# Performance work log

Hardware: AMD Instinct MI355X
Metric: run time of the kernel (lower is better)

## Reference

```python
import jax, jax.numpy as jnp
from jax import lax
import numpy as np

# Straight-through-estimator sign (standard BNN binarization):
# fwd: sign(x) with sign(0)=+1; bwd: pass gradient where |x|<=1 (hardtanh STE).
@jax.custom_vjp
def sign_ste(x):
    return jnp.where(x >= 0, 1.0, -1.0).astype(x.dtype)

def _sign_fwd(x):
    return sign_ste(x), x

def _sign_bwd(x, g):
    return (g * (jnp.abs(x) <= 1.0).astype(g.dtype),)

sign_ste.defvjp(_sign_fwd, _sign_bwd)

EPS = 1e-5  # BatchNorm eps (torch default)

def bn4(x, g, b):  # BatchNorm2d, training-mode batch stats, x: [N,C,H,W]
    m = x.mean((0, 2, 3), keepdims=True)
    v = x.var((0, 2, 3), keepdims=True)
    return g[None, :, None, None] * (x - m) * lax.rsqrt(v + EPS) + b[None, :, None, None]

def bn1(x, g, b):  # BatchNorm1d, x: [N,C]
    m = x.mean(0, keepdims=True)
    v = x.var(0, keepdims=True)
    return g * (x - m) * lax.rsqrt(v + EPS) + b

def bconv(x, W, b, first):
    # BinarizedConv2d: binarize weights always; binarize input except first layer.
    xb = x if first else sign_ste(x)
    y = lax.conv_general_dilated(xb, sign_ste(W), (1, 1), [(1, 1), (1, 1)],
                                 dimension_numbers=('NCHW', 'OIHW', 'NCHW'))
    return y + b[None, :, None, None]

def maxpool2(x):
    return lax.reduce_window(x, -jnp.inf, lax.max, (1, 1, 2, 2), (1, 1, 2, 2), 'VALID')

def ht(x):  # Hardtanh
    return jnp.clip(x, -1.0, 1.0)

CONV_CH = [(3, 64), (64, 128), (128, 256), (256, 256), (256, 512), (512, 512), (512, 512), (512, 512)]
LIN_CH = [(512, 512), (512, 512), (512, 10)]
POOL_AFTER = (0, 1, 3, 5, 7)  # conv indices followed by MaxPool2d

def setup_inputs():
    key = jax.random.key(0)
    ks = iter(jax.random.split(key, 64))
    d = {"x": jax.random.normal(next(ks), (256, 3, 32, 32), jnp.float32)}
    for i, (ci, co) in enumerate(CONV_CH):
        d[f"cw{i}"] = jax.random.normal(next(ks), (co, ci, 3, 3), jnp.float32) * 0.1
        d[f"cb{i}"] = jnp.zeros((co,), jnp.float32)
        d[f"cg{i}"] = jnp.ones((co,), jnp.float32)
        d[f"ct{i}"] = jnp.zeros((co,), jnp.float32)
    for i, (ci, co) in enumerate(LIN_CH):
        d[f"lw{i}"] = jax.random.normal(next(ks), (co, ci), jnp.float32) * 0.1
        d[f"lb{i}"] = jnp.zeros((co,), jnp.float32)
        d[f"lg{i}"] = jnp.ones((co,), jnp.float32)
        d[f"lt{i}"] = jnp.zeros((co,), jnp.float32)
    return d

def _forward(x, cw, cb, cg, ct, lw, lb, lg, lt):
    h = x
    for i in range(8):
        h = bconv(h, cw[i], cb[i], i == 0)
        if i in POOL_AFTER:
            h = maxpool2(h)
        h = ht(bn4(h, cg[i], ct[i]))
    h = h.reshape(h.shape[0], -1)  # [N, 512] after 5 pools on 32x32
    for i in range(3):
        h = sign_ste(h) @ sign_ste(lw[i]).T + lb[i]  # BinarizedLinear
        h = bn1(h, lg[i], lt[i])
        if i < 2:
            h = ht(h)  # Dropout is identity in eval mode
    return jax.nn.log_softmax(h, axis=-1)

def reference(x,
              cw0, cb0, cg0, ct0, cw1, cb1, cg1, ct1, cw2, cb2, cg2, ct2,
              cw3, cb3, cg3, ct3, cw4, cb4, cg4, ct4, cw5, cb5, cg5, ct5,
              cw6, cb6, cg6, ct6, cw7, cb7, cg7, ct7,
              lw0, lb0, lg0, lt0, lw1, lb1, lg1, lt1, lw2, lb2, lg2, lt2):
    cw = [cw0, cw1, cw2, cw3, cw4, cw5, cw6, cw7]
    cb = [cb0, cb1, cb2, cb3, cb4, cb5, cb6, cb7]
    cg = [cg0, cg1, cg2, cg3, cg4, cg5, cg6, cg7]
    ct = [ct0, ct1, ct2, ct3, ct4, ct5, ct6, ct7]
    lw = [lw0, lw1, lw2]
    lb = [lb0, lb1, lb2]
    lg = [lg0, lg1, lg2]
    lt = [lt0, lt1, lt2]
    return _forward(x, cw, cb, cg, ct, lw, lb, lg, lt)
```

## Files before the change

### kernel.cpp

```cpp
#include <hip/hip_runtime.h>
#include <hip/hip_bf16.h>

typedef unsigned long long u64;

#define EPSV 1e-5

__device__ __forceinline__ int imax(int a, int b) { return a > b ? a : b; }
__device__ __forceinline__ int iclamp(int v, int lo, int hi) { return v < lo ? lo : (v > hi ? hi : v); }

struct PrepArgs {
    const float* src[10];
    u64* dst[10];
    int CW[10];
    int Co[10];
    int taps[10];
    int rowbase[11];
    u64* accs;
    int naccs;
};

__global__ __launch_bounds__(256) void prep_kernel(PrepArgs a) {
    __shared__ float buf[4608];
    const int blk = blockIdx.x;
    int z = blk * 18 + threadIdx.x;
    if (threadIdx.x < 18 && z < a.naccs) a.accs[z] = 0ULL;

    int l = 0;
    while (l < 9 && blk >= a.rowbase[l + 1]) ++l;
    const int row = blk - a.rowbase[l];
    const int CW = a.CW[l];
    const int taps = a.taps[l];
    const int nf = CW * 64 * taps;
    const float* srow = a.src[l] + (size_t)row * nf;
    for (int i = threadIdx.x; i < nf; i += 256) buf[i] = srow[i];
    __syncthreads();
    const int t = threadIdx.x;
    if (t < taps * CW) {
        u64 bits = 0;
        if (taps == 9) {
            int k = t % 9, w = t / 9;
            for (int j = 0; j < 64; ++j) bits |= (u64)(buf[(w * 64 + j) * 9 + k] >= 0.f) << j;
            a.dst[l][(size_t)(k * CW + w) * a.Co[l] + row] = bits;
        } else {
            for (int j = 0; j < 64; ++j) bits |= (u64)(buf[t * 64 + j] >= 0.f) << j;
            a.dst[l][(size_t)row * CW + t] = bits;
        }
    }
}

__global__ __launch_bounds__(256) void conv0_lane(const float* __restrict__ x,
                                                  const float* __restrict__ wgt,
                                                  float* __restrict__ out,
                                                  double* __restrict__ dacc) {
    const int lane = threadIdx.x & 63;
    const int wave = threadIdx.x >> 6;
    float ws[27];
#pragma unroll
    for (int j = 0; j < 27; ++j) ws[j] = (wgt[lane * 27 + j] >= 0.f) ? 1.f : -1.f;

    const int gp0 = blockIdx.x * 32;
    const int n = gp0 >> 8;
    const int ypA = (gp0 >> 4) & 15;
    const int yb = 2 * ypA - 1;

    __shared__ float simg[3][6][34];
    const float* xb = x + (size_t)n * 3072;
    for (int t = threadIdx.x; t < 612; t += 256) {
        int ci = t / 204;
        int rem = t % 204;
        int r = rem / 34;
        int cc = rem % 34;
        int yy = yb + r;
        int xx = cc - 1;
        float v = 0.f;
        if ((unsigned)yy < 32u && (unsigned)xx < 32u) v = xb[(ci * 32 + yy) * 32 + xx];
        simg[ci][r][cc] = v;
    }
    __syncthreads();

    double s1 = 0.0, s2 = 0.0;
#pragma unroll 1
    for (int pi = 0; pi < 8; ++pi) {
        const int lp = wave * 8 + pi;
        const int gp = gp0 + lp;
        const int xp = lp & 15;
        const int rbase = 2 * (lp >> 4);
        const int cbase = 2 * xp;
        float win[3][4][4];
#pragma unroll
        for (int ci = 0; ci < 3; ++ci)
#pragma unroll
            for (int r = 0; r < 4; ++r)
#pragma unroll
                for (int c = 0; c < 4; ++c) win[ci][r][c] = simg[ci][rbase + r][cbase + c];
        float a00 = 0.f, a01 = 0.f, a10 = 0.f, a11 = 0.f;
#pragma unroll
        for (int ci = 0; ci < 3; ++ci)
#pragma unroll
            for (int ky = 0; ky < 3; ++ky)
#pragma unroll
                for (int kx = 0; kx < 3; ++kx) {
                    float wv = ws[ci * 9 + ky * 3 + kx];
                    a00 += win[ci][ky][kx] * wv;
                    a01 += win[ci][ky][kx + 1] * wv;
                    a10 += win[ci][ky + 1][kx] * wv;
                    a11 += win[ci][ky + 1][kx + 1] * wv;
                }
        float val = fmaxf(fmaxf(a00, a01), fmaxf(a10, a11));
        out[(size_t)gp * 64 + lane] = val;
        s1 += (double)val;
        s2 += (double)val * (double)val;
    }
    __shared__ double sh1[4][64], sh2[4][64];
    sh1[wave][lane] = s1;
    sh2[wave][lane] = s2;
    __syncthreads();
    if (threadIdx.x < 64) {
        double t1 = 0.0, t2 = 0.0;
#pragma unroll
        for (int r = 0; r < 4; ++r) { t1 += sh1[r][threadIdx.x]; t2 += sh2[r][threadIdx.x]; }
        double* sh = dacc + (size_t)(blockIdx.x & 7) * 1024;
        atomicAdd(&sh[2 * threadIdx.x], t1);
        atomicAdd(&sh[2 * threadIdx.x + 1], t2);
    }
}

__global__ __launch_bounds__(256) void bnpack_f(const float* __restrict__ in,
                                                const double* __restrict__ dacc,
                                                const float* __restrict__ g,
                                                const float* __restrict__ b,
                                                u64* __restrict__ act, int count) {
    __shared__ float2 sthr[64];
    if (threadIdx.x < 64) {
        int i = threadIdx.x;
        double S1 = 0.0, S2 = 0.0;
#pragma unroll
        for (int s = 0; s < 8; ++s) {
            S1 += dacc[s * 1024 + 2 * i];
            S2 += dacc[s * 1024 + 2 * i + 1];
        }
        double m = S1 / count;
        double var = S2 / count - m * m;
        double sc = (double)g[i] / sqrt(var + EPSV);
        float2 r;
        if (sc == 0.0) r = make_float2(b[i] >= 0.f ? -3.0e38f : 3.0e38f, 1.f);
        else {
            double t = m - (double)b[i] / sc;
            r = make_float2((float)t, sc > 0.0 ? 1.f : -1.f);
        }
        sthr[i] = r;
    }
    __syncthreads();
    int idx = blockIdx.x * 256 + threadIdx.x;
    const float4* r4 = (const float4*)(in + (size_t)idx * 64);
    u64 bits = 0;
#pragma unroll
    for (int q = 0; q < 16; ++q) {
        float4 v = r4[q];
        float vv[4] = {v.x, v.y, v.z, v.w};
#pragma unroll
        for (int u = 0; u < 4; ++u) {
            int c = q * 4 + u;
            float2 t = sthr[c];
            bool bit = (t.y > 0.f) ? (vv[u] >= t.x) : (vv[u] <= t.x);
            bits |= (u64)bit << c;
        }
    }
    act[idx] = bits;
}

__global__ __launch_bounds__(256) void bnpack_i(const short* __restrict__ in,
                                                const u64* __restrict__ iacc,
                                                const float* __restrict__ g,
                                                const float* __restrict__ b,
                                                u64* __restrict__ act, int Co, int wshift,
                                                int count) {
    __shared__ int2 sthr[520];
    for (int i = threadIdx.x; i < Co; i += 256) {
        long long S1 = 0, S2 = 0;
#pragma unroll
        for (int s = 0; s < 8; ++s) {
            S1 += (long long)iacc[s * 1024 + 2 * i];
            S2 += (long long)iacc[s * 1024 + 2 * i + 1];
        }
        double m = (double)S1 / count;
        double var = (double)S2 / count - m * m;
        double sc = (double)g[i] / sqrt(var + EPSV);
        int2 r;
        if (sc == 0.0) r = make_int2(b[i] >= 0.f ? (int)0x80000000 : 0x7fffffff, 0);
        else {
            double t = m - (double)b[i] / sc;
            if (t > 1.0e9) t = 1.0e9;
            if (t < -1.0e9) t = -1.0e9;
            r = (sc > 0.0) ? make_int2((int)ceil(t), 0) : make_int2((int)floor(t), 1);
        }
        sthr[(i >> 6) * 65 + (i & 63)] = r;
    }
    __syncthreads();
    int tid = blockIdx.x * 256 + threadIdx.x;
    int w = tid & ((1 << wshift) - 1);
    int pix = tid >> wshift;
    const int4* r4 = (const int4*)(in + (size_t)pix * Co + (w << 6));
    u64 bits = 0;
#pragma unroll
    for (int q = 0; q < 8; ++q) {
        int4 v = r4[q];
        int words[4] = {v.x, v.y, v.z, v.w};
#pragma unroll
        for (int u = 0; u < 4; ++u) {
#pragma unroll
            for (int h = 0; h < 2; ++h) {
                int c = q * 8 + u * 2 + h;
                int val = (int)(short)((h == 0) ? (words[u] & 0xffff) : ((unsigned)words[u] >> 16));
                int2 t = sthr[w * 65 + c];
                bool bit = t.y ? (val <= t.x) : (val >= t.x);
                bits |= (u64)bit << c;
            }
        }
    }
    act[tid] = bits;
}

template <int CW, int HIN, bool POOL, int PPW>
__global__ __launch_bounds__(256) void bconv_lane(const u64* __restrict__ in,
                                                  const u64* __restrict__ wpkT,
                                                  short* __restrict__ out,
                                                  u64* __restrict__ iacc, int Co) {
    constexpr int HP = POOL ? HIN / 2 : HIN;
    constexpr int NPP = HP * HP;
    constexpr int WS = POOL ? 4 : 3;
    constexpr int NA = POOL ? 4 : 1;
    const int lane = threadIdx.x & 63;
    const int wave = threadIdx.x >> 6;
    const int co = blockIdx.y * 64 + lane;

    u64 wgt[9 * CW];
#pragma unroll
    for (int j = 0; j < 9 * CW; ++j) wgt[j] = wpkT[(size_t)j * Co + co];

    int s1 = 0;
    long long s2 = 0;
    const int gp0 = (blockIdx.x * 4 + wave) * PPW;
#pragma unroll 1
    for (int pi = 0; pi < PPW; ++pi) {
        const int gp = gp0 + pi;
        const int n = gp / NPP;
        const int pp = gp % NPP;
        const int yp = pp / HP, xp = pp % HP;
        const int y0 = (POOL ? 2 * yp : yp) - 1;
        const int x0 = (POOL ? 2 * xp : xp) - 1;
        const u64* inb = in + (size_t)n * (HIN * HIN * CW);

        int offc[WS][WS];
        bool vld[WS][WS];
#pragma unroll
        for (int r = 0; r < WS; ++r) {
            int yy = y0 + r;
            int yyc = iclamp(yy, 0, HIN - 1);
#pragma unroll
            for (int c = 0; c < WS; ++c) {
                int xx = x0 + c;
                int xxc = iclamp(xx, 0, HIN - 1);
                offc[r][c] = (yyc * HIN + xxc) * CW;
                vld[r][c] = (yy == yyc) && (xx == xxc);
            }
        }

        int acc[NA];
#pragma unroll
        for (int i = 0; i < NA; ++i) acc[i] = 0;

#pragma unroll
        for (int w = 0; w < CW; ++w) {
            u64 win[WS][WS];
#pragma unroll
            for (int r = 0; r < WS; ++r)
#pragma unroll
                for (int c = 0; c < WS; ++c) win[r][c] = inb[offc[r][c] + w];
            if constexpr (POOL) {
#pragma unroll
                for (int py = 0; py < 2; ++py)
#pragma unroll
                    for (int px = 0; px < 2; ++px)
#pragma unroll
                        for (int ky = 0; ky < 3; ++ky)
#pragma unroll
                            for (int kx = 0; kx < 3; ++kx) {
                                int pcv = 64 - 2 * (int)__popcll(win[py + ky][px + kx] ^
                                                                 wgt[(ky * 3 + kx) * CW + w]);
                                acc[py * 2 + px] += vld[py + ky][px + kx] ? pcv : 0;
                            }
            } else {
#pragma unroll
                for (int ky = 0; ky < 3; ++ky)
#pragma unroll
                    for (int kx = 0; kx < 3; ++kx) {
                        int pcv = 64 - 2 * (int)__popcll(win[ky][kx] ^ wgt[(ky * 3 + kx) * CW + w]);
                        acc[0] += vld[ky][kx] ? pcv : 0;
                    }
            }
        }
        int ival;
        if constexpr (POOL)
            ival = imax(imax(acc[0], acc[1]), imax(acc[2], acc[3]));
        else
            ival = acc[0];
        out[(size_t)gp * Co + co] = (short)ival;
        s1 += ival;
        s2 += (long long)ival * ival;
    }

    __shared__ u64 sacc[128];
    if (threadIdx.x < 128) sacc[threadIdx.x] = 0ULL;
    __syncthreads();
    atomicAdd(&sacc[lane], (u64)(long long)s1);
    atomicAdd(&sacc[64 + lane], (u64)s2);
    __syncthreads();
    u64* sh = iacc + (size_t)(blockIdx.x & 7) * 1024;
    if (threadIdx.x < 64)
        atomicAdd(&sh[2 * (blockIdx.y * 64 + threadIdx.x)], sacc[threadIdx.x]);
    else if (threadIdx.x < 128)
        atomicAdd(&sh[2 * (blockIdx.y * 64 + threadIdx.x - 64) + 1], sacc[threadIdx.x]);
}

template <int CW, int HIN, bool POOL>
__global__ __launch_bounds__(256) void bconv_tiny(const u64* __restrict__ in,
                                                  const u64* __restrict__ wpkT,
                                                  short* __restrict__ out,
                                                  u64* __restrict__ iacc, int Co) {
    constexpr int NPX = HIN * HIN;
    constexpr int HP = POOL ? HIN / 2 : HIN;
    const int lane = threadIdx.x & 63;
    const int co = blockIdx.y * 64 + lane;
    const int n = blockIdx.x * 4 + (threadIdx.x >> 6);
    const u64* inb = in + (size_t)n * CW * NPX;
    int acc[NPX];
#pragma unroll
    for (int i = 0; i < NPX; ++i) acc[i] = 0;

#pragma unroll 1
    for (int w = 0; w < CW; ++w) {
        u64 win[NPX];
#pragma unroll
        for (int i = 0; i < NPX; ++i) win[i] = inb[i * CW + w];
#pragma unroll
        for (int k = 0; k < 9; ++k) {
            u64 wb = wpkT[(size_t)(k * CW + w) * Co + co];
            const int ky = k / 3, kx = k % 3;
#pragma unroll
            for (int py = 0; py < HIN; ++py)
#pragma unroll
                for (int px = 0; px < HIN; ++px) {
                    const int yy = py + ky - 1, xx = px + kx - 1;
                    if (yy >= 0 && yy < HIN && xx >= 0 && xx < HIN)
                        acc[py * HIN + px] += 64 - 2 * (int)__popcll(win[yy * HIN + xx] ^ wb);
                }
        }
    }

    short vals[HP * HP];
    if constexpr (POOL) {
#pragma unroll
        for (int py = 0; py < HP; ++py)
#pragma unroll
            for (int px = 0; px < HP; ++px)
                vals[py * HP + px] = (short)imax(
                    imax(acc[(2 * py) * HIN + 2 * px], acc[(2 * py) * HIN + 2 * px + 1]),
                    imax(acc[(2 * py + 1) * HIN + 2 * px], acc[(2 * py + 1) * HIN + 2 * px + 1]));
    } else {
#pragma unroll
        for (int i = 0; i < NPX; ++i) vals[i] = (short)acc[i];
    }
#pragma unroll
    for (int p = 0; p < HP * HP; ++p) out[(size_t)(n * HP * HP + p) * Co + co] = vals[p];

    long long s1 = 0, s2 = 0;
#pragma unroll
    for (int p = 0; p < HP * HP; ++p) {
        s1 += vals[p];
        s2 += (long long)vals[p] * vals[p];
    }
    __shared__ u64 sacc[128];
    if (threadIdx.x < 128) sacc[threadIdx.x] = 0ULL;
    __syncthreads();
    atomicAdd(&sacc[lane], (u64)s1);
    atomicAdd(&sacc[64 + lane], (u64)s2);
    __syncthreads();
    u64* sh = iacc + (size_t)(blockIdx.x & 7) * 1024;
    if (threadIdx.x < 64)
        atomicAdd(&sh[2 * (blockIdx.y * 64 + threadIdx.x)], sacc[threadIdx.x]);
    else if (threadIdx.x < 128)
        atomicAdd(&sh[2 * (blockIdx.y * 64 + threadIdx.x - 64) + 1], sacc[threadIdx.x]);
}

__global__ __launch_bounds__(256) void lin_kernel(const u64* __restrict__ hp,
                                                  const u64* __restrict__ wp,
                                                  const float* __restrict__ lb,
                                                  const float* __restrict__ g,
                                                  const float* __restrict__ bta,
                                                  float* __restrict__ z, int O, int applyHt) {
    int o = blockIdx.x;
    int n = threadIdx.x;
    const u64* hr = hp + n * 8;
    const u64* wr = wp + o * 8;
    int s = 0;
#pragma unroll
    for (int w = 0; w < 8; ++w) s += (int)__popcll(hr[w] ^ wr[w]);
    float val = (float)(512 - 2 * s) + lb[o];
    __shared__ double sh1[256], sh2[256];
    sh1[n] = (double)val;
    sh2[n] = (double)val * (double)val;
    __syncthreads();
    for (int st = 128; st > 0; st >>= 1) {
        if (n < st) {
            sh1[n] += sh1[n + st];
            sh2[n] += sh2[n + st];
        }
        __syncthreads();
    }
    __shared__ float sm, siv;
    if (n == 0) {
        double m = sh1[0] / 256.0;
        double var = sh2[0] / 256.0 - m * m;
        sm = (float)m;
        siv = (float)(1.0 / sqrt(var + EPSV));
    }
    __syncthreads();
    float zz = g[o] * (val - sm) * siv + bta[o];
    if (applyHt) zz = fminf(1.f, fmaxf(-1.f, zz));
    z[(size_t)n * O + o] = zz;
}

__global__ void pack_rows(const float* __restrict__ z, u64* __restrict__ hp) {
    int idx = blockIdx.x * 256 + threadIdx.x;
    if (idx >= 2048) return;
    int ww = idx & 7;
    int n = idx >> 3;
    u64 bits = 0;
    const float* row = z + (size_t)n * 512 + (ww << 6);
    for (int j = 0; j < 64; ++j) bits |= (u64)(row[j] >= 0.f) << j;
    hp[idx] = bits;
}

__global__ void lsm_kernel(const float* __restrict__ z, float* __restrict__ out) {
    int n = blockIdx.x * 64 + threadIdx.x;
    if (n >= 256) return;
    float v[10];
    float m = -1e30f;
#pragma unroll
    for (int i = 0; i < 10; ++i) {
        v[i] = z[n * 10 + i];
        m = fmaxf(m, v[i]);
    }
    float s = 0.f;
#pragma unroll
    for (int i = 0; i < 10; ++i) s += expf(v[i] - m);
    float ls = logf(s);
#pragma unroll
    for (int i = 0; i < 10; ++i) out[n * 10 + i] = v[i] - m - ls;
}

extern "C" void kernel_launch(void* const* d_in, const int* in_sizes, int n_in, void* d_out,
                              int out_size, void* d_ws, size_t ws_size, hipStream_t stream) {
    (void)in_sizes; (void)n_in; (void)out_size; (void)ws_size;
    const float* x = (const float*)d_in[0];
    const float *cw[8], *cb[8], *cg[8], *ct[8];
    for (int i = 0; i < 8; ++i) {
        cw[i] = (const float*)d_in[1 + 4 * i];
        cb[i] = (const float*)d_in[2 + 4 * i];
        cg[i] = (const float*)d_in[3 + 4 * i];
        ct[i] = (const float*)d_in[4 + 4 * i];
    }
    const float *lw[3], *lb[3], *lg[3], *lt[3];
    for (int i = 0; i < 3; ++i) {
        lw[i] = (const float*)d_in[33 + 4 * i];
        lb[i] = (const float*)d_in[34 + 4 * i];
        lg[i] = (const float*)d_in[35 + 4 * i];
        lt[i] = (const float*)d_in[36 + 4 * i];
    }

    static const int CIs[8] = {3, 64, 128, 256, 256, 512, 512, 512};
    static const int COs[8] = {64, 128, 256, 256, 512, 512, 512, 512};
    static const int HPs[8] = {16, 8, 8, 4, 4, 2, 2, 1};

    char* ws = (char*)d_ws;
    size_t off = 0;
    auto alloc = [&](size_t bytes) -> void* {
        void* p = ws + off;
        off += (bytes + 255) & ~(size_t)255;
        return p;
    };

    u64* wpkT[8] = {};
    for (int i = 1; i < 8; ++i) wpkT[i] = (u64*)alloc((size_t)COs[i] * 9 * (CIs[i] / 64) * 8);
    u64* wpl[3];
    int LO[3] = {512, 512, 10};
    for (int i = 0; i < 3; ++i) wpl[i] = (u64*)alloc((size_t)LO[i] * 8 * 8);
    u64* act[8];
    for (int i = 0; i < 8; ++i) act[i] = (u64*)alloc((size_t)256 * (COs[i] / 64) * HPs[i] * HPs[i] * 8);
    u64* fcs0 = (u64*)alloc(2048 * 8);
    u64* fcs1 = (u64*)alloc(2048 * 8);
    float* out0 = (float*)alloc((size_t)65536 * 64 * 4);
    short* i16A = (short*)alloc((size_t)16384 * 256 * 2);
    short* i16B = (short*)alloc((size_t)16384 * 256 * 2);
    float* z0 = (float*)alloc((size_t)256 * 512 * 4);
    float* z1 = (float*)alloc((size_t)256 * 512 * 4);
    float* z2 = (float*)alloc((size_t)256 * 10 * 4);
    u64* accs = (u64*)alloc((size_t)8 * 8 * 1024 * 8);
    double* dacc0 = (double*)accs;
    auto iacc = [&](int layer) { return accs + (size_t)layer * 8192; };

    PrepArgs pa;
    int rb = 0;
    for (int i = 1; i < 8; ++i) {
        int e = i - 1;
        pa.src[e] = cw[i];
        pa.dst[e] = wpkT[i];
        pa.CW[e] = CIs[i] / 64;
        pa.Co[e] = COs[i];
        pa.taps[e] = 9;
        pa.rowbase[e] = rb;
        rb += COs[i];
    }
    for (int i = 0; i < 3; ++i) {
        int e = 7 + i;
        pa.src[e] = lw[i];
        pa.dst[e] = wpl[i];
        pa.CW[e] = 8;
        pa.Co[e] = LO[i];
        pa.taps[e] = 1;
        pa.rowbase[e] = rb;
        rb += LO[i];
    }
    pa.rowbase[10] = rb;
    pa.accs = accs;
    pa.naccs = 8 * 8 * 1024;
    prep_kernel<<<rb, 256, 0, stream>>>(pa);

    conv0_lane<<<2048, 256, 0, stream>>>(x, cw[0], out0, dacc0);
    bnpack_f<<<256, 256, 0, stream>>>(out0, dacc0, cg[0], ct[0], act[0], 65536);

    bconv_lane<1, 16, true, 4><<<dim3(1024, 2), 256, 0, stream>>>(act[0], wpkT[1], i16A, iacc(1), 128);
    bnpack_i<<<128, 256, 0, stream>>>(i16A, iacc(1), cg[1], ct[1], act[1], 128, 1, 16384);

    bconv_lane<2, 8, false, 4><<<dim3(1024, 4), 256, 0, stream>>>(act[1], wpkT[2], i16B, iacc(2), 256);
    bnpack_i<<<256, 256, 0, stream>>>(i16B, iacc(2), cg[2], ct[2], act[2], 256, 2, 16384);

    bconv_lane<4, 8, true, 2><<<dim3(512, 4), 256, 0, stream>>>(act[2], wpkT[3], i16A, iacc(3), 256);
    bnpack_i<<<64, 256, 0, stream>>>(i16A, iacc(3), cg[3], ct[3], act[3], 256, 2, 4096);

    bconv_lane<4, 4, false, 2><<<dim3(512, 8), 256, 0, stream>>>(act[3], wpkT[4], i16B, iacc(4), 512);
    bnpack_i<<<128, 256, 0, stream>>>(i16B, iacc(4), cg[4], ct[4], act[4], 512, 3, 4096);

    bconv_tiny<8, 4, true><<<dim3(64, 8), 256, 0, stream>>>(act[4], wpkT[5], i16A, iacc(5), 512);
    bnpack_i<<<32, 256, 0, stream>>>(i16A, iacc(5), cg[5], ct[5], act[5], 512, 3, 1024);

    bconv_tiny<8, 2, false><<<dim3(64, 8), 256, 0, stream>>>(act[5], wpkT[6], i16B, iacc(6), 512);
    bnpack_i<<<32, 256, 0, stream>>>(i16B, iacc(6), cg[6], ct[6], act[6], 512, 3, 1024);

    bconv_tiny<8, 2, true><<<dim3(64, 8), 256, 0, stream>>>(act[6], wpkT[7], i16A, iacc(7), 512);
    bnpack_i<<<8, 256, 0, stream>>>(i16A, iacc(7), cg[7], ct[7], act[7], 512, 3, 256);

    lin_kernel<<<512, 256, 0, stream>>>(act[7], wpl[0], lb[0], lg[0], lt[0], z0, 512, 1);
    pack_rows<<<8, 256, 0, stream>>>(z0, fcs0);
    lin_kernel<<<512, 256, 0, stream>>>(fcs0, wpl[1], lb[1], lg[1], lt[1], z1, 512, 1);
    pack_rows<<<8, 256, 0, stream>>>(z1, fcs1);
    lin_kernel<<<10, 256, 0, stream>>>(fcs1, wpl[2], lb[2], lg[2], lt[2], z2, 10, 0);
    lsm_kernel<<<4, 64, 0, stream>>>(z2, (float*)d_out);
}
```

Before: 473.4 us.

## Pad packed activations with zero halo and correct borders via weight sums

Packed bit activations for layers 1-3 are now written into buffers with a one-pixel halo, which the prep kernel zeroes. This removes the per-tap clamping and validity masks from the binary conv inner loop. Border pixels are fixed after accumulation by subtracting precomputed per-tap weight sums, since a zero word XORs to the weight's popcount. The change also adds 128-bit vector loads for multi-word channels, fully unrolls the pixel loop and halves pixels per wave while doubling the grid. The costs are extra zeroing work, larger buffers and more register pressure from the unrolling.

```diff
diff --git a/kernel.cpp b/kernel.cpp
--- a/kernel.cpp
+++ b/kernel.cpp
@@ -6,7 +6,6 @@
 #define EPSV 1e-5
 
 __device__ __forceinline__ int imax(int a, int b) { return a > b ? a : b; }
-__device__ __forceinline__ int iclamp(int v, int lo, int hi) { return v < lo ? lo : (v > hi ? hi : v); }
 
 struct PrepArgs {
     const float* src[10];
@@ -15,15 +14,15 @@
     int Co[10];
     int taps[10];
     int rowbase[11];
-    u64* accs;
-    int naccs;
+    u64* zptr;
+    int nzero;
 };
 
 __global__ __launch_bounds__(256) void prep_kernel(PrepArgs a) {
     __shared__ float buf[4608];
     const int blk = blockIdx.x;
-    int z = blk * 18 + threadIdx.x;
-    if (threadIdx.x < 18 && z < a.naccs) a.accs[z] = 0ULL;
+    int z = blk * 256 + threadIdx.x;
+    if (z < a.nzero) a.zptr[z] = 0ULL;
 
     int l = 0;
     while (l < 9 && blk >= a.rowbase[l + 1]) ++l;
@@ -166,15 +165,17 @@
             bits |= (u64)bit << c;
         }
     }
-    act[idx] = bits;
-}
-
+    int n = idx >> 8, yp = (idx >> 4) & 15, xp = idx & 15;
+    act[(size_t)(n * 18 + yp + 1) * 18 + xp + 1] = bits;
+}
+
+template <int HALO>
 __global__ __launch_bounds__(256) void bnpack_i(const short* __restrict__ in,
                                                 const u64* __restrict__ iacc,
                                                 const float* __restrict__ g,
                                                 const float* __restrict__ b,
                                                 u64* __restrict__ act, int Co, int wshift,
-                                                int count) {
+                                                int hpshift, int SH, int count) {
     __shared__ int2 sthr[520];
     for (int i = threadIdx.x; i < Co; i += 256) {
         long long S1 = 0, S2 = 0;
@@ -218,14 +219,23 @@
             }
         }
     }
-    act[tid] = bits;
-}
-
-template <int CW, int HIN, bool POOL, int PPW>
+    if (HALO) {
+        int HP = 1 << hpshift;
+        int n = pix >> (2 * hpshift);
+        int p = pix & ((1 << (2 * hpshift)) - 1);
+        int yp = p >> hpshift, xp = p & (HP - 1);
+        act[((size_t)((n * SH + yp + 1) * SH + xp + 1) << wshift) + w] = bits;
+    } else {
+        act[tid] = bits;
+    }
+}
+
+template <int CW, int HIN, bool POOL, int PPW, int WC>
 __global__ __launch_bounds__(256) void bconv_lane(const u64* __restrict__ in,
                                                   const u64* __restrict__ wpkT,
                                                   short* __restrict__ out,
                                                   u64* __restrict__ iacc, int Co) {
+    constexpr int H2 = HIN + 2;
     constexpr int HP = POOL ? HIN / 2 : HIN;
     constexpr int NPP = HP * HP;
     constexpr int WS = POOL ? 4 : 3;
@@ -237,74 +247,113 @@
     u64 wgt[9 * CW];
 #pragma unroll
     for (int j = 0; j < 9 * CW; ++j) wgt[j] = wpkT[(size_t)j * Co + co];
+    int C[9];
+#pragma unroll
+    for (int k = 0; k < 9; ++k) {
+        int s = 0;
+#pragma unroll
+        for (int w = 0; w < CW; ++w) s += 64 - 2 * (int)__popcll(wgt[k * CW + w]);
+        C[k] = s;
+    }
 
     int s1 = 0;
     long long s2 = 0;
     const int gp0 = (blockIdx.x * 4 + wave) * PPW;
-#pragma unroll 1
+#pragma unroll
     for (int pi = 0; pi < PPW; ++pi) {
         const int gp = gp0 + pi;
         const int n = gp / NPP;
         const int pp = gp % NPP;
         const int yp = pp / HP, xp = pp % HP;
-        const int y0 = (POOL ? 2 * yp : yp) - 1;
-        const int x0 = (POOL ? 2 * xp : xp) - 1;
-        const u64* inb = in + (size_t)n * (HIN * HIN * CW);
-
-        int offc[WS][WS];
-        bool vld[WS][WS];
-#pragma unroll
-        for (int r = 0; r < WS; ++r) {
-            int yy = y0 + r;
-            int yyc = iclamp(yy, 0, HIN - 1);
-#pragma unroll
-            for (int c = 0; c < WS; ++c) {
-                int xx = x0 + c;
-                int xxc = iclamp(xx, 0, HIN - 1);
-                offc[r][c] = (yyc * HIN + xxc) * CW;
-                vld[r][c] = (yy == yyc) && (xx == xxc);
+        const int yb = POOL ? 2 * yp : yp;
+        const int xb = POOL ? 2 * xp : xp;
+        const u64* inb = in + (size_t)n * (H2 * H2 * CW);
+
+        int acc[NA];
+#pragma unroll
+        for (int i = 0; i < NA; ++i) acc[i] = 0;
+
+#pragma unroll
+        for (int w0 = 0; w0 < CW; w0 += WC) {
+            u64 win[WS][WS][WC];
+#pragma unroll
+            for (int r = 0; r < WS; ++r)
+#pragma unroll
+                for (int c = 0; c < WS; ++c) {
+                    const u64* p = inb + ((size_t)(yb + r) * H2 + (xb + c)) * CW + w0;
+                    if (WC == 1) {
+                        win[r][c][0] = p[0];
+                    } else {
+                        ulonglong2 v = *(const ulonglong2*)p;
+                        win[r][c][0] = v.x;
+                        win[r][c][1] = v.y;
+                    }
+                }
+#pragma unroll
+            for (int w = 0; w < WC; ++w) {
+                if constexpr (POOL) {
+#pragma unroll
+                    for (int py = 0; py < 2; ++py)
+#pragma unroll
+                        for (int px = 0; px < 2; ++px)
+#pragma unroll
+                            for (int ky = 0; ky < 3; ++ky)
+#pragma unroll
+                                for (int kx = 0; kx < 3; ++kx)
+                                    acc[py * 2 + px] +=
+                                        64 - 2 * (int)__popcll(win[py + ky][px + kx][w] ^
+                                                               wgt[(ky * 3 + kx) * CW + w0 + w]);
+                } else {
+#pragma unroll
+                    for (int ky = 0; ky < 3; ++ky)
+#pragma unroll
+                        for (int kx = 0; kx < 3; ++kx)
+                            acc[0] += 64 - 2 * (int)__popcll(win[ky][kx][w] ^
+                                                             wgt[(ky * 3 + kx) * CW + w0 + w]);
+                }
             }
         }
 
-        int acc[NA];
-#pragma unroll
-        for (int i = 0; i < NA; ++i) acc[i] = 0;
-
-#pragma unroll
-        for (int w = 0; w < CW; ++w) {
-            u64 win[WS][WS];
-#pragma unroll
-            for (int r = 0; r < WS; ++r)
-#pragma unroll
-                for (int c = 0; c < WS; ++c) win[r][c] = inb[offc[r][c] + w];
+        const bool interior = POOL ? (yp > 0 && yp < HP - 1 && xp > 0 && xp < HP - 1)
+                                   : (yp > 0 && yp < HIN - 1 && xp > 0 && xp < HIN - 1);
+        int v[NA];
+        if (interior) {
+#pragma unroll
+            for (int i = 0; i < NA; ++i) v[i] = acc[i];
+        } else {
+            bool rp[WS], cp[WS];
+#pragma unroll
+            for (int r = 0; r < WS; ++r) rp[r] = ((unsigned)(yb + r - 1) >= (unsigned)HIN);
+#pragma unroll
+            for (int c = 0; c < WS; ++c) cp[c] = ((unsigned)(xb + c - 1) >= (unsigned)HIN);
             if constexpr (POOL) {
 #pragma unroll
                 for (int py = 0; py < 2; ++py)
 #pragma unroll
-                    for (int px = 0; px < 2; ++px)
+                    for (int px = 0; px < 2; ++px) {
+                        int corr = 0;
 #pragma unroll
                         for (int ky = 0; ky < 3; ++ky)
 #pragma unroll
-                            for (int kx = 0; kx < 3; ++kx) {
-                                int pcv = 64 - 2 * (int)__popcll(win[py + ky][px + kx] ^
-                                                                 wgt[(ky * 3 + kx) * CW + w]);
-                                acc[py * 2 + px] += vld[py + ky][px + kx] ? pcv : 0;
-                            }
+                            for (int kx = 0; kx < 3; ++kx)
+                                if (rp[py + ky] || cp[px + kx]) corr += C[ky * 3 + kx];
+                        v[py * 2 + px] = acc[py * 2 + px] - corr;
+                    }
             } else {
+                int corr = 0;
 #pragma unroll
                 for (int ky = 0; ky < 3; ++ky)
 #pragma unroll
-                    for (int kx = 0; kx < 3; ++kx) {
-                        int pcv = 64 - 2 * (int)__popcll(win[ky][kx] ^ wgt[(ky * 3 + kx) * CW + w]);
-                        acc[0] += vld[ky][kx] ? pcv : 0;
-                    }
+                    for (int kx = 0; kx < 3; ++kx)
+                        if (rp[ky] || cp[kx]) corr += C[ky * 3 + kx];
+                v[0] = acc[0] - corr;
             }
         }
         int ival;
         if constexpr (POOL)
-            ival = imax(imax(acc[0], acc[1]), imax(acc[2], acc[3]));
+            ival = imax(imax(v[0], v[1]), imax(v[2], v[3]));
         else
-            ival = acc[0];
+            ival = v[0];
         out[(size_t)gp * Co + co] = (short)ival;
         s1 += ival;
         s2 += (long long)ival * ival;
@@ -481,7 +530,6 @@
 
     static const int CIs[8] = {3, 64, 128, 256, 256, 512, 512, 512};
     static const int COs[8] = {64, 128, 256, 256, 512, 512, 512, 512};
-    static const int HPs[8] = {16, 8, 8, 4, 4, 2, 2, 1};
 
     char* ws = (char*)d_ws;
     size_t off = 0;
@@ -496,8 +544,17 @@
     u64* wpl[3];
     int LO[3] = {512, 512, 10};
     for (int i = 0; i < 3; ++i) wpl[i] = (u64*)alloc((size_t)LO[i] * 8 * 8);
-    u64* act[8];
-    for (int i = 0; i < 8; ++i) act[i] = (u64*)alloc((size_t)256 * (COs[i] / 64) * HPs[i] * HPs[i] * 8);
+
+    u64* accs = (u64*)alloc((size_t)8 * 8 * 1024 * 8);
+    u64* actH = (u64*)alloc((size_t)273408 * 8);
+    u64* act0 = actH;
+    u64* act1 = actH + 82944;
+    u64* act2 = actH + 134144;
+    u64* act3 = actH + 236544;
+    u64* act4 = (u64*)alloc((size_t)256 * 16 * 8 * 8);
+    u64* act5 = (u64*)alloc((size_t)256 * 4 * 8 * 8);
+    u64* act6 = (u64*)alloc((size_t)256 * 4 * 8 * 8);
+    u64* act7 = (u64*)alloc((size_t)256 * 1 * 8 * 8);
     u64* fcs0 = (u64*)alloc(2048 * 8);
     u64* fcs1 = (u64*)alloc(2048 * 8);
     float* out0 = (float*)alloc((size_t)65536 * 64 * 4);
@@ -506,7 +563,6 @@
     float* z0 = (float*)alloc((size_t)256 * 512 * 4);
     float* z1 = (float*)alloc((size_t)256 * 512 * 4);
     float* z2 = (float*)alloc((size_t)256 * 10 * 4);
-    u64* accs = (u64*)alloc((size_t)8 * 8 * 1024 * 8);
     double* dacc0 = (double*)accs;
     auto iacc = [&](int layer) { return accs + (size_t)layer * 8192; };
 
@@ -533,35 +589,35 @@
         rb += LO[i];
     }
     pa.rowbase[10] = rb;
-    pa.accs = accs;
-    pa.naccs = 8 * 8 * 1024;
+    pa.zptr = accs;
+    pa.nzero = 65536 + 273408;
     prep_kernel<<<rb, 256, 0, stream>>>(pa);
 
     conv0_lane<<<2048, 256, 0, stream>>>(x, cw[0], out0, dacc0);
-    bnpack_f<<<256, 256, 0, stream>>>(out0, dacc0, cg[0], ct[0], act[0], 65536);
-
-    bconv_lane<1, 16, true, 4><<<dim3(1024, 2), 256, 0, stream>>>(act[0], wpkT[1], i16A, iacc(1), 128);
-    bnpack_i<<<128, 256, 0, stream>>>(i16A, iacc(1), cg[1], ct[1], act[1], 128, 1, 16384);
-
-    bconv_lane<2, 8, false, 4><<<dim3(1024, 4), 256, 0, stream>>>(act[1], wpkT[2], i16B, iacc(2), 256);
-    bnpack_i<<<256, 256, 0, stream>>>(i16B, iacc(2), cg[2], ct[2], act[2], 256, 2, 16384);
-
-    bconv_lane<4, 8, true, 2><<<dim3(512, 4), 256, 0, stream>>>(act[2], wpkT[3], i16A, iacc(3), 256);
-    bnpack_i<<<64, 256, 0, stream>>>(i16A, iacc(3), cg[3], ct[3], act[3], 256, 2, 4096);
-
-    bconv_lane<4, 4, false, 2><<<dim3(512, 8), 256, 0, stream>>>(act[3], wpkT[4], i16B, iacc(4), 512);
-    bnpack_i<<<128, 256, 0, stream>>>(i16B, iacc(4), cg[4], ct[4], act[4], 512, 3, 4096);
-
-    bconv_tiny<8, 4, true><<<dim3(64, 8), 256, 0, stream>>>(act[4], wpkT[5], i16A, iacc(5), 512);
-    bnpack_i<<<32, 256, 0, stream>>>(i16A, iacc(5), cg[5], ct[5], act[5], 512, 3, 1024);
-
-    bconv_tiny<8, 2, false><<<dim3(64, 8), 256, 0, stream>>>(act[5], wpkT[6], i16B, iacc(6), 512);
-    bnpack_i<<<32, 256, 0, stream>>>(i16B, iacc(6), cg[6], ct[6], act[6], 512, 3, 1024);
-
-    bconv_tiny<8, 2, true><<<dim3(64, 8), 256, 0, stream>>>(act[6], wpkT[7], i16A, iacc(7), 512);
-    bnpack_i<<<8, 256, 0, stream>>>(i16A, iacc(7), cg[7], ct[7], act[7], 512, 3, 256);
-
-    lin_kernel<<<512, 256, 0, stream>>>(act[7], wpl[0], lb[0], lg[0], lt[0], z0, 512, 1);
+    bnpack_f<<<256, 256, 0, stream>>>(out0, dacc0, cg[0], ct[0], act0, 65536);
+
+    bconv_lane<1, 16, true, 2, 1><<<dim3(2048, 2), 256, 0, stream>>>(act0, wpkT[1], i16A, iacc(1), 128);
+    bnpack_i<1><<<128, 256, 0, stream>>>(i16A, iacc(1), cg[1], ct[1], act1, 128, 1, 3, 10, 16384);
+
+    bconv_lane<2, 8, false, 2, 2><<<dim3(2048, 4), 256, 0, stream>>>(act1, wpkT[2], i16B, iacc(2), 256);
+    bnpack_i<1><<<256, 256, 0, stream>>>(i16B, iacc(2), cg[2], ct[2], act2, 256, 2, 3, 10, 16384);
+
+    bconv_lane<4, 8, true, 1, 2><<<dim3(1024, 4), 256, 0, stream>>>(act2, wpkT[3], i16A, iacc(3), 256);
+    bnpack_i<1><<<64, 256, 0, stream>>>(i16A, iacc(3), cg[3], ct[3], act3, 256, 2, 2, 6, 4096);
+
+    bconv_lane<4, 4, false, 1, 2><<<dim3(1024, 8), 256, 0, stream>>>(act3, wpkT[4], i16B, iacc(4), 512);
+    bnpack_i<0><<<128, 256, 0, stream>>>(i16B, iacc(4), cg[4], ct[4], act4, 512, 3, 2, 0, 4096);
+
+    bconv_tiny<8, 4, true><<<dim3(64, 8), 256, 0, stream>>>(act4, wpkT[5], i16A, iacc(5), 512);
+    bnpack_i<0><<<32, 256, 0, stream>>>(i16A, iacc(5), cg[5], ct[5], act5, 512, 3, 1, 0, 1024);
+
+    bconv_tiny<8, 2, false><<<dim3(64, 8), 256, 0, stream>>>(act5, wpkT[6], i16B, iacc(6), 512);
+    bnpack_i<0><<<32, 256, 0, stream>>>(i16B, iacc(6), cg[6], ct[6], act6, 512, 3, 1, 0, 1024);
+
+    bconv_tiny<8, 2, true><<<dim3(64, 8), 256, 0, stream>>>(act6, wpkT[7], i16A, iacc(7), 512);
+    bnpack_i<0><<<8, 256, 0, stream>>>(i16A, iacc(7), cg[7], ct[7], act7, 512, 3, 0, 0, 256);
+
+    lin_kernel<<<512, 256, 0, stream>>>(act7, wpl[0], lb[0], lg[0], lt[0], z0, 512, 1);
     pack_rows<<<8, 256, 0, stream>>>(z0, fcs0);
     lin_kernel<<<512, 256, 0, stream>>>(fcs0, wpl[1], lb[1], lg[1], lt[1], z1, 512, 1);
     pack_rows<<<8, 256, 0, stream>>>(z1, fcs1);
```

Result: slower. 577.8 us (+22.0%).

## Process a full output row per wave with sliding input window reuse

Applied to the files above, without the earlier changes.

Replaces the per-pixel binary conv kernel with a row-based kernel where each wave computes an entire output row. A sliding register window along x loads only the new columns for each step, so neighbouring pixels reuse input words. Weights are loaded in chunks of channel words instead of all at once. Interior rows take a specialised path that drops the row-validity selects. The larger per-thread accumulator array and fully unrolled row loop raise register pressure and can lower occupancy, and the grids are halved.

```diff
diff --git a/kernel.cpp b/kernel.cpp
--- a/kernel.cpp
+++ b/kernel.cpp
@@ -221,91 +221,178 @@
     act[tid] = bits;
 }
 
-template <int CW, int HIN, bool POOL, int PPW>
-__global__ __launch_bounds__(256) void bconv_lane(const u64* __restrict__ in,
-                                                  const u64* __restrict__ wpkT,
-                                                  short* __restrict__ out,
-                                                  u64* __restrict__ iacc, int Co) {
+template <int CW, int HIN, bool POOL, int WC, bool INTERIOR>
+__device__ __forceinline__ void row_accum(const u64* __restrict__ inb,
+                                          const u64* __restrict__ wpkT, int Co, int co,
+                                          const int* yoff, const bool* ry, int* acc) {
     constexpr int HP = POOL ? HIN / 2 : HIN;
-    constexpr int NPP = HP * HP;
+    constexpr int WS = POOL ? 4 : 3;
+    constexpr int NA = POOL ? 4 : 1;
+#pragma unroll 1
+    for (int w0 = 0; w0 < CW; w0 += WC) {
+        u64 wg[9 * WC];
+#pragma unroll
+        for (int k = 0; k < 9; ++k)
+#pragma unroll
+            for (int w = 0; w < WC; ++w)
+                wg[k * WC + w] = wpkT[(size_t)(k * CW + w0 + w) * Co + co];
+        u64 cur[WS][WS][WC];
+#pragma unroll
+        for (int d = 0; d < WS; ++d) {
+            int cc = d - 1;
+            int ccc = cc < 0 ? 0 : cc;
+#pragma unroll
+            for (int r = 0; r < WS; ++r) {
+                const u64* p = inb + yoff[r] + ccc * CW + w0;
+                if (WC == 1) {
+                    cur[r][d][0] = p[0];
+                } else {
+                    ulonglong2 v = *(const ulonglong2*)p;
+                    cur[r][d][0] = v.x;
+                    cur[r][d][1] = v.y;
+                }
+            }
+        }
+#pragma unroll
+        for (int xp = 0; xp < HP; ++xp) {
+            if constexpr (POOL) {
+#pragma unroll
+                for (int py = 0; py < 2; ++py)
+#pragma unroll
+                    for (int qx = 0; qx < 2; ++qx)
+#pragma unroll
+                        for (int ky = 0; ky < 3; ++ky)
+#pragma unroll
+                            for (int kx = 0; kx < 3; ++kx) {
+                                int d = qx + kx;
+                                int cc = 2 * xp + d - 1;
+                                if (cc >= 0 && cc < HIN) {
+#pragma unroll
+                                    for (int w = 0; w < WC; ++w) {
+                                        int pcv = 64 - 2 * (int)__popcll(cur[py + ky][d][w] ^
+                                                                         wg[(ky * 3 + kx) * WC + w]);
+                                        if constexpr (INTERIOR)
+                                            acc[xp * NA + py * 2 + qx] += pcv;
+                                        else
+                                            acc[xp * NA + py * 2 + qx] += ry[py + ky] ? pcv : 0;
+                                    }
+                                }
+                            }
+            } else {
+#pragma unroll
+                for (int ky = 0; ky < 3; ++ky)
+#pragma unroll
+                    for (int kx = 0; kx < 3; ++kx) {
+                        int cc = xp + kx - 1;
+                        if (cc >= 0 && cc < HIN) {
+#pragma unroll
+                            for (int w = 0; w < WC; ++w) {
+                                int pcv = 64 - 2 * (int)__popcll(cur[ky][kx][w] ^
+                                                                 wg[(ky * 3 + kx) * WC + w]);
+                                if constexpr (INTERIOR)
+                                    acc[xp] += pcv;
+                                else
+                                    acc[xp] += ry[ky] ? pcv : 0;
+                            }
+                        }
+                    }
+            }
+            if (xp < HP - 1) {
+                if constexpr (POOL) {
+#pragma unroll
+                    for (int r = 0; r < WS; ++r)
+#pragma unroll
+                        for (int w = 0; w < WC; ++w) {
+                            cur[r][0][w] = cur[r][2][w];
+                            cur[r][1][w] = cur[r][3][w];
+                        }
+#pragma unroll
+                    for (int dd = 2; dd < 4; ++dd) {
+                        int cc = 2 * (xp + 1) + dd - 1;
+                        int ccc = cc >= HIN ? HIN - 1 : cc;
+#pragma unroll
+                        for (int r = 0; r < WS; ++r) {
+                            const u64* p = inb + yoff[r] + ccc * CW + w0;
+                            if (WC == 1) {
+                                cur[r][dd][0] = p[0];
+                            } else {
+                                ulonglong2 v = *(const ulonglong2*)p;
+                                cur[r][dd][0] = v.x;
+                                cur[r][dd][1] = v.y;
+                            }
+                        }
+                    }
+                } else {
+#pragma unroll
+                    for (int r = 0; r < WS; ++r)
+#pragma unroll
+                        for (int w = 0; w < WC; ++w) {
+                            cur[r][0][w] = cur[r][1][w];
+                            cur[r][1][w] = cur[r][2][w];
+                        }
+                    int cc = xp + 2;
+                    int ccc = cc >= HIN ? HIN - 1 : cc;
+#pragma unroll
+                    for (int r = 0; r < WS; ++r) {
+                        const u64* p = inb + yoff[r] + ccc * CW + w0;
+                        if (WC == 1) {
+                            cur[r][2][0] = p[0];
+                        } else {
+                            ulonglong2 v = *(const ulonglong2*)p;
+                            cur[r][2][0] = v.x;
+                            cur[r][2][1] = v.y;
+                        }
+                    }
+                }
+            }
+        }
+    }
+}
+
+template <int CW, int HIN, bool POOL, int WC>
+__global__ __launch_bounds__(256) void bconv_row(const u64* __restrict__ in,
+                                                 const u64* __restrict__ wpkT,
+                                                 short* __restrict__ out,
+                                                 u64* __restrict__ iacc, int Co) {
+    constexpr int HP = POOL ? HIN / 2 : HIN;
     constexpr int WS = POOL ? 4 : 3;
     constexpr int NA = POOL ? 4 : 1;
     const int lane = threadIdx.x & 63;
-    const int wave = threadIdx.x >> 6;
     const int co = blockIdx.y * 64 + lane;
-
-    u64 wgt[9 * CW];
-#pragma unroll
-    for (int j = 0; j < 9 * CW; ++j) wgt[j] = wpkT[(size_t)j * Co + co];
+    const int grow = blockIdx.x * 4 + (threadIdx.x >> 6);
+    const int n = grow / HP;
+    const int yp = grow % HP;
+    const int y0 = (POOL ? 2 * yp : yp) - 1;
+    const u64* inb = in + (size_t)n * (HIN * HIN * CW);
+    int yoff[WS];
+    bool ry[WS];
+#pragma unroll
+    for (int r = 0; r < WS; ++r) {
+        int y = y0 + r;
+        ry[r] = (unsigned)y < (unsigned)HIN;
+        int yc = iclamp(y, 0, HIN - 1);
+        yoff[r] = yc * HIN * CW;
+    }
+    int acc[HP * NA];
+#pragma unroll
+    for (int i = 0; i < HP * NA; ++i) acc[i] = 0;
+
+    if (yp > 0 && yp < HP - 1)
+        row_accum<CW, HIN, POOL, WC, true>(inb, wpkT, Co, co, yoff, ry, acc);
+    else
+        row_accum<CW, HIN, POOL, WC, false>(inb, wpkT, Co, co, yoff, ry, acc);
 
     int s1 = 0;
     long long s2 = 0;
-    const int gp0 = (blockIdx.x * 4 + wave) * PPW;
-#pragma unroll 1
-    for (int pi = 0; pi < PPW; ++pi) {
-        const int gp = gp0 + pi;
-        const int n = gp / NPP;
-        const int pp = gp % NPP;
-        const int yp = pp / HP, xp = pp % HP;
-        const int y0 = (POOL ? 2 * yp : yp) - 1;
-        const int x0 = (POOL ? 2 * xp : xp) - 1;
-        const u64* inb = in + (size_t)n * (HIN * HIN * CW);
-
-        int offc[WS][WS];
-        bool vld[WS][WS];
-#pragma unroll
-        for (int r = 0; r < WS; ++r) {
-            int yy = y0 + r;
-            int yyc = iclamp(yy, 0, HIN - 1);
-#pragma unroll
-            for (int c = 0; c < WS; ++c) {
-                int xx = x0 + c;
-                int xxc = iclamp(xx, 0, HIN - 1);
-                offc[r][c] = (yyc * HIN + xxc) * CW;
-                vld[r][c] = (yy == yyc) && (xx == xxc);
-            }
-        }
-
-        int acc[NA];
-#pragma unroll
-        for (int i = 0; i < NA; ++i) acc[i] = 0;
-
-#pragma unroll
-        for (int w = 0; w < CW; ++w) {
-            u64 win[WS][WS];
-#pragma unroll
-            for (int r = 0; r < WS; ++r)
-#pragma unroll
-                for (int c = 0; c < WS; ++c) win[r][c] = inb[offc[r][c] + w];
-            if constexpr (POOL) {
-#pragma unroll
-                for (int py = 0; py < 2; ++py)
-#pragma unroll
-                    for (int px = 0; px < 2; ++px)
-#pragma unroll
-                        for (int ky = 0; ky < 3; ++ky)
-#pragma unroll
-                            for (int kx = 0; kx < 3; ++kx) {
-                                int pcv = 64 - 2 * (int)__popcll(win[py + ky][px + kx] ^
-                                                                 wgt[(ky * 3 + kx) * CW + w]);
-                                acc[py * 2 + px] += vld[py + ky][px + kx] ? pcv : 0;
-                            }
-            } else {
-#pragma unroll
-                for (int ky = 0; ky < 3; ++ky)
-#pragma unroll
-                    for (int kx = 0; kx < 3; ++kx) {
-                        int pcv = 64 - 2 * (int)__popcll(win[ky][kx] ^ wgt[(ky * 3 + kx) * CW + w]);
-                        acc[0] += vld[ky][kx] ? pcv : 0;
-                    }
-            }
-        }
+    short* orow = out + (size_t)grow * HP * Co + co;
+#pragma unroll
+    for (int xp = 0; xp < HP; ++xp) {
         int ival;
         if constexpr (POOL)
-            ival = imax(imax(acc[0], acc[1]), imax(acc[2], acc[3]));
+            ival = imax(imax(acc[xp * 4], acc[xp * 4 + 1]), imax(acc[xp * 4 + 2], acc[xp * 4 + 3]));
         else
-            ival = acc[0];
-        out[(size_t)gp * Co + co] = (short)ival;
+            ival = acc[xp];
+        orow[(size_t)xp * Co] = (short)ival;
         s1 += ival;
         s2 += (long long)ival * ival;
     }
@@ -540,16 +627,16 @@
     conv0_lane<<<2048, 256, 0, stream>>>(x, cw[0], out0, dacc0);
     bnpack_f<<<256, 256, 0, stream>>>(out0, dacc0, cg[0], ct[0], act[0], 65536);
 
-    bconv_lane<1, 16, true, 4><<<dim3(1024, 2), 256, 0, stream>>>(act[0], wpkT[1], i16A, iacc(1), 128);
+    bconv_row<1, 16, true, 1><<<dim3(512, 2), 256, 0, stream>>>(act[0], wpkT[1], i16A, iacc(1), 128);
     bnpack_i<<<128, 256, 0, stream>>>(i16A, iacc(1), cg[1], ct[1], act[1], 128, 1, 16384);
 
-    bconv_lane<2, 8, false, 4><<<dim3(1024, 4), 256, 0, stream>>>(act[1], wpkT[2], i16B, iacc(2), 256);
+    bconv_row<2, 8, false, 2><<<dim3(512, 4), 256, 0, stream>>>(act[1], wpkT[2], i16B, iacc(2), 256);
     bnpack_i<<<256, 256, 0, stream>>>(i16B, iacc(2), cg[2], ct[2], act[2], 256, 2, 16384);
 
-    bconv_lane<4, 8, true, 2><<<dim3(512, 4), 256, 0, stream>>>(act[2], wpkT[3], i16A, iacc(3), 256);
+    bconv_row<4, 8, true, 2><<<dim3(256, 4), 256, 0, stream>>>(act[2], wpkT[3], i16A, iacc(3), 256);
     bnpack_i<<<64, 256, 0, stream>>>(i16A, iacc(3), cg[3], ct[3], act[3], 256, 2, 4096);
 
-    bconv_lane<4, 4, false, 2><<<dim3(512, 8), 256, 0, stream>>>(act[3], wpkT[4], i16B, iacc(4), 512);
+    bconv_row<4, 4, false, 2><<<dim3(256, 8), 256, 0, stream>>>(act[3], wpkT[4], i16B, iacc(4), 512);
     bnpack_i<<<128, 256, 0, stream>>>(i16B, iacc(4), cg[4], ct[4], act[4], 512, 3, 4096);
 
     bconv_tiny<8, 4, true><<<dim3(64, 8), 256, 0, stream>>>(act[4], wpkT[5], i16A, iacc(5), 512);
```

Result: faster. 404.0 us (-14.7%).
